# Kernel tuning notes

Hardware: AMD Instinct MI355X
Metric: run time of the kernel (lower is better)

Reference implementation:

```python
import jax, jax.numpy as jnp
import numpy as np

B, C, N, K, OUT = 4, 64, 4096, 20, 64  # batch, feat dim, points, neighbors, out channels
EPS = 1e-5  # InstanceNorm2d default eps
NEG_SLOPE = 0.2


def setup_inputs() -> dict:
    key = jax.random.key(0)
    k1, k2 = jax.random.split(key)
    points = jax.random.normal(k1, (B, C, N), dtype=jnp.float32)
    W = jax.random.normal(k2, (OUT, 2 * C), dtype=jnp.float32) * 0.05  # 1x1 conv weight, no bias
    return {"points": points, "W": W}


def reference(points, W):
    # points: [B, C, N]
    xt = jnp.swapaxes(points, 1, 2)                       # [B, N, C]
    sq = jnp.sum(xt * xt, axis=-1)                        # [B, N]
    inner = jnp.einsum('bnc,bmc->bnm', xt, xt)            # [B, N, N]
    neg_dist = 2.0 * inner - sq[:, :, None] - sq[:, None, :]  # -||x_i - x_j||^2
    _, idx = jax.lax.top_k(neg_dist, K)                   # [B, N, K] nearest neighbors (incl. self)

    # gather neighbor features: [B, N, K, C]
    feat_j = jax.vmap(lambda t, i: t[i])(xt, idx)
    feat_i = xt[:, :, None, :]                            # [B, N, 1, C]
    edge = jnp.concatenate(
        [feat_j - feat_i, jnp.broadcast_to(feat_i, feat_j.shape)], axis=-1
    )                                                     # [B, N, K, 2C]

    # 1x1 conv == per-edge matmul
    y = jnp.einsum('bnkc,oc->bnko', edge, W)              # [B, N, K, OUT]

    # InstanceNorm2d: normalize over spatial dims (N, K) per (batch, channel)
    mean = jnp.mean(y, axis=(1, 2), keepdims=True)
    var = jnp.var(y, axis=(1, 2), keepdims=True)
    y = (y - mean) * jax.lax.rsqrt(var + EPS)

    # LeakyReLU(0.2)
    y = jnp.where(y >= 0, y, NEG_SLOPE * y)

    # max-pool over neighbors
    y = jnp.max(y, axis=2)                                # [B, N, OUT]
    return jnp.swapaxes(y, 1, 2)                          # [B, OUT, N]
```

## Files before the change

kernel.cpp:

```cpp
#include <hip/hip_runtime.h>
#include <math.h>

#define B_    4
#define N_    4096
#define K_    20
#define EPS_  1e-5f
#define NSL_  0.2f
#define MARGIN_ 0.05f
#define QCAP  64

typedef _Float16 h8 __attribute__((ext_vector_type(8)));
typedef float    f4 __attribute__((ext_vector_type(4)));

#define GLD16(gp, lp) __builtin_amdgcn_global_load_lds( \
    (const __attribute__((address_space(1))) void*)(gp), \
    (__attribute__((address_space(3))) void*)(lp), 16, 0, 0)
#define GLD4(gp, lp) __builtin_amdgcn_global_load_lds( \
    (const __attribute__((address_space(1))) void*)(gp), \
    (__attribute__((address_space(3))) void*)(lp), 4, 0, 0)

__global__ void prep_kernel(const float* __restrict__ pts,
                            h8* __restrict__ Xh, h8* __restrict__ Xl,
                            float* __restrict__ sq) {
    int gid = blockIdx.x * 256 + threadIdx.x;
    int b = gid >> 12, n = gid & 4095;
    const float* p = pts + (size_t)b * 64 * 4096 + n;
    float s = 0.f;
#pragma unroll
    for (int g = 0; g < 8; ++g) {
        h8 hh, ll;
#pragma unroll
        for (int i = 0; i < 8; ++i) {
            float x = p[(size_t)(g * 8 + i) * 4096];
            s = fmaf(x, x, s);
            _Float16 h = (_Float16)x;
            hh[i] = h;
            ll[i] = (_Float16)(x - (float)h);
        }
        Xh[(size_t)(b * 8 + g) * 4096 + n] = hh;
        Xl[(size_t)(b * 8 + g) * 4096 + n] = ll;
    }
    sq[gid] = s;
}

__device__ __forceinline__ void topk_insert(float (&tv)[20], int (&ti)[20], float v, int ix) {
    if (v > tv[19] || (v == tv[19] && ix < ti[19])) {
        tv[19] = v; ti[19] = ix;
#pragma unroll
        for (int p = 19; p > 0; --p) {
            bool sw = (tv[p] > tv[p - 1]) || (tv[p] == tv[p - 1] && ti[p] < ti[p - 1]);
            float av = tv[p - 1]; int ai = ti[p - 1];
            float bv = tv[p];     int bi = ti[p];
            tv[p - 1] = sw ? bv : av;  ti[p - 1] = sw ? bi : ai;
            tv[p]     = sw ? av : bv;  ti[p]     = sw ? ai : bi;
        }
    }
}

__global__ __launch_bounds__(256) void knn4_kernel(
        const h8* __restrict__ Xh, const h8* __restrict__ Xl,
        const float* __restrict__ sqa, int* __restrict__ idxo) {
    __shared__ __align__(16) char smem[58880];
    h8*    jHs  = (h8*)(smem);
    h8*    jLs  = (h8*)(smem + 16384);
    h8*    qHs  = (h8*)(smem + 32768);
    h8*    qLs  = (h8*)(smem + 36864);
    float* xqe  = (float*)(smem + 40960);
    float* sqjl = (float*)(smem + 49664);
    float* tauv = (float*)(smem + 50176);
    int*   qcnt = (int*)  (smem + 50304);
    int*   qix  = (int*)  (smem + 50432);
    float* coll = (float*)(smem);
    float* qval = (float*)(smem);

    int t    = threadIdx.x;
    int lane = t & 63, w = t >> 6;
    int c15  = lane & 15, g4 = lane >> 4;
    int b    = blockIdx.x >> 7;
    int q0   = (blockIdx.x & 127) << 5;
    const h8* XhB = Xh + (size_t)b * 8 * 4096;
    const h8* XlB = Xl + (size_t)b * 8 * 4096;
    const float* sqg = sqa + b * 4096;

    {
        int g = t >> 5, q = t & 31;
        qHs[g * 32 + q] = XhB[(size_t)g * 4096 + q0 + q];
        qLs[g * 32 + q] = XlB[(size_t)g * 4096 + q0 + q];
    }
    __syncthreads();
#pragma unroll
    for (int s = 0; s < 8; ++s) {
        int idx = s * 256 + t;
        int q = idx >> 6, c = idx & 63;
        xqe[q * 68 + c] = (float)qHs[(c >> 3) * 32 + q][c & 7]
                        + (float)qLs[(c >> 3) * 32 + q][c & 7];
    }

    auto stage = [&](int nb, int jb) {
        GLD16(XhB + (size_t)w       * 4096 + jb + lane, jHs + nb * 512 + w       * 64);
        GLD16(XhB + (size_t)(w + 4) * 4096 + jb + lane, jHs + nb * 512 + (w + 4) * 64);
        GLD16(XlB + (size_t)w       * 4096 + jb + lane, jLs + nb * 512 + w       * 64);
        GLD16(XlB + (size_t)(w + 4) * 4096 + jb + lane, jLs + nb * 512 + (w + 4) * 64);
        if (w == 0) GLD4(sqg + jb + lane, sqjl + nb * 64);
    };

    f4 a0, a1;
    auto sweep = [&](int cur) {
        a0 = (f4){0.f, 0.f, 0.f, 0.f};
        a1 = (f4){0.f, 0.f, 0.f, 0.f};
#pragma unroll
        for (int kc = 0; kc < 2; ++kc) {
            int g = kc * 4 + g4;
            h8 bh  = jHs[cur * 512 + g * 64 + w * 16 + c15];
            h8 bl  = jLs[cur * 512 + g * 64 + w * 16 + c15];
            h8 qh0 = qHs[g * 32 + c15];
            h8 ql0 = qLs[g * 32 + c15];
            h8 qh1 = qHs[g * 32 + 16 + c15];
            h8 ql1 = qLs[g * 32 + 16 + c15];
            a0 = __builtin_amdgcn_mfma_f32_16x16x32_f16(qh0, bh, a0, 0, 0, 0);
            a0 = __builtin_amdgcn_mfma_f32_16x16x32_f16(qh0, bl, a0, 0, 0, 0);
            a0 = __builtin_amdgcn_mfma_f32_16x16x32_f16(ql0, bh, a0, 0, 0, 0);
            a1 = __builtin_amdgcn_mfma_f32_16x16x32_f16(qh1, bh, a1, 0, 0, 0);
            a1 = __builtin_amdgcn_mfma_f32_16x16x32_f16(qh1, bl, a1, 0, 0, 0);
            a1 = __builtin_amdgcn_mfma_f32_16x16x32_f16(ql1, bh, a1, 0, 0, 0);
        }
    };

    float t0v[2][4], t1v[2][4];
#pragma unroll
    for (int qs = 0; qs < 2; ++qs)
#pragma unroll
        for (int r = 0; r < 4; ++r) { t0v[qs][r] = -INFINITY; t1v[qs][r] = -INFINITY; }

    stage(0, 0);
    __syncthreads();
    for (int step = 0; step < 64; ++step) {
        int cur = step & 1;
        if (step < 63) stage(cur ^ 1, (step + 1) * 64);
        sweep(cur);
        float sj = sqjl[cur * 64 + w * 16 + c15];
#pragma unroll
        for (int r = 0; r < 4; ++r) {
            float v0 = 2.f * a0[r] - sj;
            t1v[0][r] = fminf(t0v[0][r], fmaxf(t1v[0][r], v0));
            t0v[0][r] = fmaxf(t0v[0][r], v0);
            float v1 = 2.f * a1[r] - sj;
            t1v[1][r] = fminf(t0v[1][r], fmaxf(t1v[1][r], v1));
            t0v[1][r] = fmaxf(t0v[1][r], v1);
        }
        __syncthreads();
    }

    int s0 = w * 32 + c15 * 2;
#pragma unroll
    for (int qs = 0; qs < 2; ++qs)
#pragma unroll
        for (int r = 0; r < 4; ++r) {
            int q = qs * 16 + g4 * 4 + r;
            coll[(s0 + 0) * 33 + q] = t0v[qs][r];
            coll[(s0 + 1) * 33 + q] = t1v[qs][r];
        }
    __syncthreads();
    if (t < 32) {
        float tv[20];
#pragma unroll
        for (int p = 0; p < 20; ++p) tv[p] = -INFINITY;
#pragma unroll 1
        for (int s = 0; s < 128; ++s) {
            float v = coll[s * 33 + t];
            if (v > tv[19]) {
                tv[19] = v;
#pragma unroll
                for (int p = 19; p > 0; --p) {
                    float a = tv[p - 1], bb = tv[p];
                    tv[p - 1] = fmaxf(a, bb);
                    tv[p]     = fminf(a, bb);
                }
            }
        }
        tauv[t] = tv[19] - MARGIN_;
        qcnt[t] = 0;
    }
    __syncthreads();

    float taur[2][4];
#pragma unroll
    for (int qs = 0; qs < 2; ++qs)
#pragma unroll
        for (int r = 0; r < 4; ++r)
            taur[qs][r] = tauv[qs * 16 + g4 * 4 + r];

    stage(0, 0);
    __syncthreads();
    for (int step = 0; step < 64; ++step) {
        int cur = step & 1;
        if (step < 63) stage(cur ^ 1, (step + 1) * 64);
        sweep(cur);
        float sj = sqjl[cur * 64 + w * 16 + c15];
        int jg = step * 64 + w * 16 + c15;
#pragma unroll
        for (int r = 0; r < 4; ++r) {
            float v0 = 2.f * a0[r] - sj;
            if (v0 >= taur[0][r]) {
                int q = g4 * 4 + r;
                int p = atomicAdd(&qcnt[q], 1);
                if (p < QCAP) qix[p * 33 + q] = jg;
            }
            float v1 = 2.f * a1[r] - sj;
            if (v1 >= taur[1][r]) {
                int q = 16 + g4 * 4 + r;
                int p = atomicAdd(&qcnt[q], 1);
                if (p < QCAP) qix[p * 33 + q] = jg;
            }
        }
        __syncthreads();
    }

    {
        int q = t >> 3;
        int cnt = qcnt[q]; if (cnt > QCAP) cnt = QCAP;
        for (int p = t & 7; p < cnt; p += 8) {
            int j = qix[p * 33 + q];
            float s = 0.f;
#pragma unroll
            for (int g = 0; g < 8; ++g) {
                h8 jh = XhB[(size_t)g * 4096 + j];
                h8 jl = XlB[(size_t)g * 4096 + j];
#pragma unroll
                for (int i = 0; i < 8; ++i) {
                    float xj = (float)jh[i] + (float)jl[i];
                    s = fmaf(xqe[q * 68 + g * 8 + i], xj, s);
                }
            }
            qval[p * 33 + q] = 2.f * s - sqg[j];
        }
    }
    __syncthreads();

    if (t < 32) {
        int cnt = qcnt[t]; if (cnt > QCAP) cnt = QCAP;
        float tv[20]; int ti[20];
#pragma unroll
        for (int p = 0; p < 20; ++p) { tv[p] = -INFINITY; ti[p] = 0x7fffffff; }
#pragma unroll 1
        for (int p = 0; p < cnt; ++p)
            topk_insert(tv, ti, qval[p * 33 + t], qix[p * 33 + t]);
#pragma unroll
        for (int p = 0; p < 20; ++p)
            idxo[((size_t)(b * 4096 + q0 + t)) * 20 + p] = ti[p];
    }
}

__global__ void ugemm_kernel(const float* __restrict__ pts, const float* __restrict__ W,
                             float* __restrict__ u1, float* __restrict__ u2) {
    __shared__ float W1l[64 * 65];
    __shared__ float W2l[64 * 65];
    int t  = threadIdx.x;
    int b  = blockIdx.x >> 6;
    int j0 = (blockIdx.x & 63) << 6;
    int o  = t & 63, jg = t >> 6;

#pragma unroll
    for (int s = 0; s < 16; ++s) {
        int lin = s * 256 + t;
        int oo = lin >> 6, c = lin & 63;
        float w1 = W[oo * 128 + c];
        W1l[oo * 65 + c] = w1;
        W2l[oo * 65 + c] = W[oo * 128 + 64 + c] - w1;
    }
    __syncthreads();

    float acc1[16], acc2[16];
#pragma unroll
    for (int jj = 0; jj < 16; ++jj) { acc1[jj] = 0.f; acc2[jj] = 0.f; }

    const float* pbj = pts + (size_t)b * 64 * 4096 + j0 + jg * 16;
#pragma unroll 4
    for (int c = 0; c < 64; ++c) {
        float w1 = W1l[o * 65 + c];
        float w2 = W2l[o * 65 + c];
#pragma unroll
        for (int jj = 0; jj < 16; ++jj) {
            float p = pbj[(size_t)c * 4096 + jj];
            acc1[jj] = fmaf(w1, p, acc1[jj]);
            acc2[jj] = fmaf(w2, p, acc2[jj]);
        }
    }
#pragma unroll
    for (int jj = 0; jj < 16; ++jj) {
        int j = j0 + jg * 16 + jj;
        u1[(size_t)(b * 4096 + j) * 64 + o] = acc1[jj];
        u2[(size_t)(b * 4096 + j) * 64 + o] = acc2[jj];
    }
}

__global__ void gather_kernel(const float* __restrict__ u1, const float* __restrict__ u2,
                              const int* __restrict__ idxi, float* __restrict__ ymax,
                              float* __restrict__ stats) {
    __shared__ float red[2 * 4 * 64];
    int t  = threadIdx.x;
    int o  = t & 63, ng = t >> 6;
    int b  = blockIdx.x >> 10;
    int n  = ((blockIdx.x & 1023) << 2) + ng;
    int bn = b * 4096 + n;

    float v2 = u2[(size_t)bn * 64 + o];
    float m = -INFINITY, s = 0.f, q = 0.f;
#pragma unroll
    for (int k = 0; k < 20; ++k) {
        int j = idxi[(size_t)bn * 20 + k];
        float y = u1[(size_t)(b * 4096 + j) * 64 + o] + v2;
        m = fmaxf(m, y);
        s += y;
        q = fmaf(y, y, q);
    }
    ymax[(size_t)bn * 64 + o] = m;
    red[ng * 64 + o] = s;
    red[256 + ng * 64 + o] = q;
    __syncthreads();
    if (t < 64) {
        float s_ = red[t] + red[64 + t] + red[128 + t] + red[192 + t];
        float q_ = red[256 + t] + red[256 + 64 + t] + red[256 + 128 + t] + red[256 + 192 + t];
        atomicAdd(&stats[b * 64 + t], s_);
        atomicAdd(&stats[256 + b * 64 + t], q_);
    }
}

__global__ void finalize_kernel(const float* __restrict__ ymax, const float* __restrict__ stats,
                                float* __restrict__ out) {
    int gid = blockIdx.x * 256 + threadIdx.x;
    int n = gid & 4095;
    int o = (gid >> 12) & 63;
    int b = gid >> 18;
    const float cnt = (float)(N_ * K_);
    float mean = stats[b * 64 + o] / cnt;
    float var  = stats[256 + b * 64 + o] / cnt - mean * mean;
    float inv  = rsqrtf(var + EPS_);
    float v = ymax[(size_t)(b * 4096 + n) * 64 + o];
    float z = (v - mean) * inv;
    out[gid] = z >= 0.f ? z : NSL_ * z;
}

extern "C" void kernel_launch(void* const* d_in, const int* in_sizes, int n_in,
                              void* d_out, int out_size, void* d_ws, size_t ws_size,
                              hipStream_t stream) {
    const float* pts = (const float*)d_in[0];
    const float* W   = (const float*)d_in[1];
    float* out = (float*)d_out;
    char* ws = (char*)d_ws;

    h8*    Xh    = (h8*)(ws);
    h8*    Xl    = (h8*)(ws + 2097152);
    float* ymax  = (float*)(ws);
    float* u1    = (float*)(ws + 4194304);
    float* u2    = (float*)(ws + 8388608);
    float* sq    = (float*)(ws + 12582912);
    int*   idx   = (int*)  (ws + 12648448);
    float* stats = (float*)(ws + 13959168);

    hipMemsetAsync(stats, 0, 512 * sizeof(float), stream);
    prep_kernel     <<<64,   256, 0, stream>>>(pts, Xh, Xl, sq);
    knn4_kernel     <<<512,  256, 0, stream>>>(Xh, Xl, sq, idx);
    ugemm_kernel    <<<256,  256, 0, stream>>>(pts, W, u1, u2);
    gather_kernel   <<<4096, 256, 0, stream>>>(u1, u2, idx, ymax, stats);
    finalize_kernel <<<4096, 256, 0, stream>>>(ymax, stats, out);
}
```

Before: 296.5 us.

## Load kNN operands directly into registers, dropping LDS staging and barriers

The kNN kernel no longer stages candidate and query tiles through shared memory with global_load_lds and a barrier every step. Each lane now loads its MFMA fragments straight from global memory into registers, one step ahead of use, and keeps the query fragments in registers for both sweeps. This removes 128 __syncthreads and shrinks LDS so more blocks fit per CU (launch_bounds 256,4). The cost is redundant global/L2 loads, since each wave loads its own fragments, plus higher register pressure.

```diff
diff --git a/kernel.cpp b/kernel.cpp
--- a/kernel.cpp
+++ b/kernel.cpp
@@ -12,12 +12,7 @@
 typedef _Float16 h8 __attribute__((ext_vector_type(8)));
 typedef float    f4 __attribute__((ext_vector_type(4)));
 
-#define GLD16(gp, lp) __builtin_amdgcn_global_load_lds( \
-    (const __attribute__((address_space(1))) void*)(gp), \
-    (__attribute__((address_space(3))) void*)(lp), 16, 0, 0)
-#define GLD4(gp, lp) __builtin_amdgcn_global_load_lds( \
-    (const __attribute__((address_space(1))) void*)(gp), \
-    (__attribute__((address_space(3))) void*)(lp), 4, 0, 0)
+#define MFMA32(A, Bv, C) __builtin_amdgcn_mfma_f32_16x16x32_f16((A), (Bv), (C), 0, 0, 0)
 
 __global__ void prep_kernel(const float* __restrict__ pts,
                             h8* __restrict__ Xh, h8* __restrict__ Xl,
@@ -57,21 +52,16 @@
     }
 }
 
-__global__ __launch_bounds__(256) void knn4_kernel(
+__global__ __launch_bounds__(256, 4) void knn5_kernel(
         const h8* __restrict__ Xh, const h8* __restrict__ Xl,
         const float* __restrict__ sqa, int* __restrict__ idxo) {
-    __shared__ __align__(16) char smem[58880];
-    h8*    jHs  = (h8*)(smem);
-    h8*    jLs  = (h8*)(smem + 16384);
-    h8*    qHs  = (h8*)(smem + 32768);
-    h8*    qLs  = (h8*)(smem + 36864);
-    float* xqe  = (float*)(smem + 40960);
-    float* sqjl = (float*)(smem + 49664);
-    float* tauv = (float*)(smem + 50176);
-    int*   qcnt = (int*)  (smem + 50304);
-    int*   qix  = (int*)  (smem + 50432);
+    __shared__ __align__(16) char smem[25856];
     float* coll = (float*)(smem);
-    float* qval = (float*)(smem);
+    float* xqe  = (float*)(smem);
+    float* qval = (float*)(smem + 8704);
+    int*   qix  = (int*)  (smem + 17152);
+    float* tauv = (float*)(smem + 25600);
+    int*   qcnt = (int*)  (smem + 25728);
 
     int t    = threadIdx.x;
     int lane = t & 63, w = t >> 6;
@@ -82,73 +72,66 @@
     const h8* XlB = Xl + (size_t)b * 8 * 4096;
     const float* sqg = sqa + b * 4096;
 
+    const h8* QHlo = XhB + (size_t)g4 * 4096 + q0;
+    const h8* QHhi = XhB + (size_t)(g4 + 4) * 4096 + q0;
+    const h8* QLlo = XlB + (size_t)g4 * 4096 + q0;
+    const h8* QLhi = XlB + (size_t)(g4 + 4) * 4096 + q0;
+    h8 qh0_lo = QHlo[c15], qh1_lo = QHlo[16 + c15];
+    h8 qh0_hi = QHhi[c15], qh1_hi = QHhi[16 + c15];
+    h8 ql0_lo = QLlo[c15], ql1_lo = QLlo[16 + c15];
+    h8 ql0_hi = QLhi[c15], ql1_hi = QLhi[16 + c15];
+
+    int jb0 = w * 16 + c15;
+    const h8* pbh_lo = XhB + (size_t)g4 * 4096 + jb0;
+    const h8* pbh_hi = XhB + (size_t)(g4 + 4) * 4096 + jb0;
+    const h8* pbl_lo = XlB + (size_t)g4 * 4096 + jb0;
+    const h8* pbl_hi = XlB + (size_t)(g4 + 4) * 4096 + jb0;
+    const float* psj = sqg + jb0;
+
+    float t0v[2][4], t1v[2][4];
+#pragma unroll
+    for (int qs = 0; qs < 2; ++qs)
+#pragma unroll
+        for (int r = 0; r < 4; ++r) { t0v[qs][r] = -INFINITY; t1v[qs][r] = -INFINITY; }
+
     {
-        int g = t >> 5, q = t & 31;
-        qHs[g * 32 + q] = XhB[(size_t)g * 4096 + q0 + q];
-        qLs[g * 32 + q] = XlB[(size_t)g * 4096 + q0 + q];
-    }
-    __syncthreads();
-#pragma unroll
-    for (int s = 0; s < 8; ++s) {
-        int idx = s * 256 + t;
-        int q = idx >> 6, c = idx & 63;
-        xqe[q * 68 + c] = (float)qHs[(c >> 3) * 32 + q][c & 7]
-                        + (float)qLs[(c >> 3) * 32 + q][c & 7];
-    }
-
-    auto stage = [&](int nb, int jb) {
-        GLD16(XhB + (size_t)w       * 4096 + jb + lane, jHs + nb * 512 + w       * 64);
-        GLD16(XhB + (size_t)(w + 4) * 4096 + jb + lane, jHs + nb * 512 + (w + 4) * 64);
-        GLD16(XlB + (size_t)w       * 4096 + jb + lane, jLs + nb * 512 + w       * 64);
-        GLD16(XlB + (size_t)(w + 4) * 4096 + jb + lane, jLs + nb * 512 + (w + 4) * 64);
-        if (w == 0) GLD4(sqg + jb + lane, sqjl + nb * 64);
-    };
-
-    f4 a0, a1;
-    auto sweep = [&](int cur) {
-        a0 = (f4){0.f, 0.f, 0.f, 0.f};
-        a1 = (f4){0.f, 0.f, 0.f, 0.f};
-#pragma unroll
-        for (int kc = 0; kc < 2; ++kc) {
-            int g = kc * 4 + g4;
-            h8 bh  = jHs[cur * 512 + g * 64 + w * 16 + c15];
-            h8 bl  = jLs[cur * 512 + g * 64 + w * 16 + c15];
-            h8 qh0 = qHs[g * 32 + c15];
-            h8 ql0 = qLs[g * 32 + c15];
-            h8 qh1 = qHs[g * 32 + 16 + c15];
-            h8 ql1 = qLs[g * 32 + 16 + c15];
-            a0 = __builtin_amdgcn_mfma_f32_16x16x32_f16(qh0, bh, a0, 0, 0, 0);
-            a0 = __builtin_amdgcn_mfma_f32_16x16x32_f16(qh0, bl, a0, 0, 0, 0);
-            a0 = __builtin_amdgcn_mfma_f32_16x16x32_f16(ql0, bh, a0, 0, 0, 0);
-            a1 = __builtin_amdgcn_mfma_f32_16x16x32_f16(qh1, bh, a1, 0, 0, 0);
-            a1 = __builtin_amdgcn_mfma_f32_16x16x32_f16(qh1, bl, a1, 0, 0, 0);
-            a1 = __builtin_amdgcn_mfma_f32_16x16x32_f16(ql1, bh, a1, 0, 0, 0);
-        }
-    };
-
-    float t0v[2][4], t1v[2][4];
-#pragma unroll
-    for (int qs = 0; qs < 2; ++qs)
-#pragma unroll
-        for (int r = 0; r < 4; ++r) { t0v[qs][r] = -INFINITY; t1v[qs][r] = -INFINITY; }
-
-    stage(0, 0);
-    __syncthreads();
-    for (int step = 0; step < 64; ++step) {
-        int cur = step & 1;
-        if (step < 63) stage(cur ^ 1, (step + 1) * 64);
-        sweep(cur);
-        float sj = sqjl[cur * 64 + w * 16 + c15];
-#pragma unroll
-        for (int r = 0; r < 4; ++r) {
-            float v0 = 2.f * a0[r] - sj;
-            t1v[0][r] = fminf(t0v[0][r], fmaxf(t1v[0][r], v0));
-            t0v[0][r] = fmaxf(t0v[0][r], v0);
-            float v1 = 2.f * a1[r] - sj;
-            t1v[1][r] = fminf(t0v[1][r], fmaxf(t1v[1][r], v1));
-            t0v[1][r] = fmaxf(t0v[1][r], v1);
-        }
-        __syncthreads();
+        h8 bh_lo = pbh_lo[0], bh_hi = pbh_hi[0];
+        h8 bl_lo = pbl_lo[0], bl_hi = pbl_hi[0];
+        float sj = psj[0];
+        for (int step = 0; step < 64; ++step) {
+            int noff = ((step < 63) ? (step + 1) : 63) * 64;
+            h8 nbh_lo = pbh_lo[noff], nbh_hi = pbh_hi[noff];
+            h8 nbl_lo = pbl_lo[noff], nbl_hi = pbl_hi[noff];
+            float nsj = psj[noff];
+
+            f4 a0 = (f4){0.f, 0.f, 0.f, 0.f};
+            f4 a1 = (f4){0.f, 0.f, 0.f, 0.f};
+            a0 = MFMA32(qh0_lo, bh_lo, a0);
+            a0 = MFMA32(qh0_lo, bl_lo, a0);
+            a0 = MFMA32(ql0_lo, bh_lo, a0);
+            a0 = MFMA32(qh0_hi, bh_hi, a0);
+            a0 = MFMA32(qh0_hi, bl_hi, a0);
+            a0 = MFMA32(ql0_hi, bh_hi, a0);
+            a1 = MFMA32(qh1_lo, bh_lo, a1);
+            a1 = MFMA32(qh1_lo, bl_lo, a1);
+            a1 = MFMA32(ql1_lo, bh_lo, a1);
+            a1 = MFMA32(qh1_hi, bh_hi, a1);
+            a1 = MFMA32(qh1_hi, bl_hi, a1);
+            a1 = MFMA32(ql1_hi, bh_hi, a1);
+
+#pragma unroll
+            for (int r = 0; r < 4; ++r) {
+                float v0 = 2.f * a0[r] - sj;
+                t1v[0][r] = fminf(t0v[0][r], fmaxf(t1v[0][r], v0));
+                t0v[0][r] = fmaxf(t0v[0][r], v0);
+                float v1 = 2.f * a1[r] - sj;
+                t1v[1][r] = fminf(t0v[1][r], fmaxf(t1v[1][r], v1));
+                t0v[1][r] = fmaxf(t0v[1][r], v1);
+            }
+            bh_lo = nbh_lo; bh_hi = nbh_hi;
+            bl_lo = nbl_lo; bl_hi = nbl_hi;
+            sj = nsj;
+        }
     }
 
     int s0 = w * 32 + c15 * 2;
@@ -183,6 +166,15 @@
     }
     __syncthreads();
 
+    {
+        int q = t >> 3, g = t & 7;
+        h8 hh = XhB[(size_t)g * 4096 + q0 + q];
+        h8 ll = XlB[(size_t)g * 4096 + q0 + q];
+#pragma unroll
+        for (int i = 0; i < 8; ++i)
+            xqe[q * 68 + g * 8 + i] = (float)hh[i] + (float)ll[i];
+    }
+
     float taur[2][4];
 #pragma unroll
     for (int qs = 0; qs < 2; ++qs)
@@ -190,31 +182,53 @@
         for (int r = 0; r < 4; ++r)
             taur[qs][r] = tauv[qs * 16 + g4 * 4 + r];
 
-    stage(0, 0);
-    __syncthreads();
-    for (int step = 0; step < 64; ++step) {
-        int cur = step & 1;
-        if (step < 63) stage(cur ^ 1, (step + 1) * 64);
-        sweep(cur);
-        float sj = sqjl[cur * 64 + w * 16 + c15];
-        int jg = step * 64 + w * 16 + c15;
-#pragma unroll
-        for (int r = 0; r < 4; ++r) {
-            float v0 = 2.f * a0[r] - sj;
-            if (v0 >= taur[0][r]) {
-                int q = g4 * 4 + r;
-                int p = atomicAdd(&qcnt[q], 1);
-                if (p < QCAP) qix[p * 33 + q] = jg;
+    {
+        h8 bh_lo = pbh_lo[0], bh_hi = pbh_hi[0];
+        h8 bl_lo = pbl_lo[0], bl_hi = pbl_hi[0];
+        float sj = psj[0];
+        for (int step = 0; step < 64; ++step) {
+            int noff = ((step < 63) ? (step + 1) : 63) * 64;
+            h8 nbh_lo = pbh_lo[noff], nbh_hi = pbh_hi[noff];
+            h8 nbl_lo = pbl_lo[noff], nbl_hi = pbl_hi[noff];
+            float nsj = psj[noff];
+
+            f4 a0 = (f4){0.f, 0.f, 0.f, 0.f};
+            f4 a1 = (f4){0.f, 0.f, 0.f, 0.f};
+            a0 = MFMA32(qh0_lo, bh_lo, a0);
+            a0 = MFMA32(qh0_lo, bl_lo, a0);
+            a0 = MFMA32(ql0_lo, bh_lo, a0);
+            a0 = MFMA32(qh0_hi, bh_hi, a0);
+            a0 = MFMA32(qh0_hi, bl_hi, a0);
+            a0 = MFMA32(ql0_hi, bh_hi, a0);
+            a1 = MFMA32(qh1_lo, bh_lo, a1);
+            a1 = MFMA32(qh1_lo, bl_lo, a1);
+            a1 = MFMA32(ql1_lo, bh_lo, a1);
+            a1 = MFMA32(qh1_hi, bh_hi, a1);
+            a1 = MFMA32(qh1_hi, bl_hi, a1);
+            a1 = MFMA32(ql1_hi, bh_hi, a1);
+
+            int jg = step * 64 + w * 16 + c15;
+#pragma unroll
+            for (int r = 0; r < 4; ++r) {
+                float v0 = 2.f * a0[r] - sj;
+                if (v0 >= taur[0][r]) {
+                    int q = g4 * 4 + r;
+                    int p = atomicAdd(&qcnt[q], 1);
+                    if (p < QCAP) qix[p * 33 + q] = jg;
+                }
+                float v1 = 2.f * a1[r] - sj;
+                if (v1 >= taur[1][r]) {
+                    int q = 16 + g4 * 4 + r;
+                    int p = atomicAdd(&qcnt[q], 1);
+                    if (p < QCAP) qix[p * 33 + q] = jg;
+                }
             }
-            float v1 = 2.f * a1[r] - sj;
-            if (v1 >= taur[1][r]) {
-                int q = 16 + g4 * 4 + r;
-                int p = atomicAdd(&qcnt[q], 1);
-                if (p < QCAP) qix[p * 33 + q] = jg;
-            }
-        }
-        __syncthreads();
-    }
+            bh_lo = nbh_lo; bh_hi = nbh_hi;
+            bl_lo = nbl_lo; bl_hi = nbl_hi;
+            sj = nsj;
+        }
+    }
+    __syncthreads();
 
     {
         int q = t >> 3;
@@ -360,7 +374,7 @@
 
     hipMemsetAsync(stats, 0, 512 * sizeof(float), stream);
     prep_kernel     <<<64,   256, 0, stream>>>(pts, Xh, Xl, sq);
-    knn4_kernel     <<<512,  256, 0, stream>>>(Xh, Xl, sq, idx);
+    knn5_kernel     <<<512,  256, 0, stream>>>(Xh, Xl, sq, idx);
     ugemm_kernel    <<<256,  256, 0, stream>>>(pts, W, u1, u2);
     gather_kernel   <<<4096, 256, 0, stream>>>(u1, u2, idx, ymax, stats);
     finalize_kernel <<<4096, 256, 0, stream>>>(ymax, stats, out);
```

Result: faster. 270.9 us (-8.6%).
